# Optimization experiments

Measured on AMD Instinct MI355X. Metric: run time of the kernel, lower is better.

Reference implementation:

```python
import jax, jax.numpy as jnp
import numpy as np
import math

D_MODEL = 64
D_STATE = 16
V_RANGE = 1
K = 3
BATCH, H, W = 4, 32, 32
V_LIST = [(x, y) for x in range(-V_RANGE, V_RANGE + 1) for y in range(-V_RANGE, V_RANGE + 1)]
NUM_V = len(V_LIST)


def _circ_conv(x, w):
    # x: (B, Cin, H, W), w: (Cout, Cin, K, K); circular padding then VALID conv
    p = K // 2
    xp = jnp.pad(x, ((0, 0), (0, 0), (p, p), (p, p)), mode='wrap')
    return jax.lax.conv_general_dilated(
        xp, w, window_strides=(1, 1), padding='VALID',
        dimension_numbers=('NCHW', 'OIHW', 'NCHW'))


def setup_inputs() -> dict:
    key = jax.random.key(0)
    ks = jax.random.split(key, 8)
    fan = 1.0 / math.sqrt(D_MODEL * K * K)
    u_t = jax.random.normal(ks[0], (BATCH, D_MODEL, H, W), dtype=jnp.float32)
    s_prev = jax.random.normal(ks[1], (BATCH, NUM_V, D_MODEL, D_STATE, H, W), dtype=jnp.float32)
    conv_delta_w = jax.random.normal(ks[2], (D_MODEL, D_MODEL, K, K), dtype=jnp.float32) * fan
    conv_delta_b = jax.random.normal(ks[3], (D_MODEL,), dtype=jnp.float32) * 0.01
    conv_B_w = jax.random.normal(ks[4], (D_STATE, D_MODEL, K, K), dtype=jnp.float32) * fan
    conv_C_w = jax.random.normal(ks[5], (D_STATE, D_MODEL, K, K), dtype=jnp.float32) * fan
    log_A_real = jnp.log(0.5 * jnp.ones((D_MODEL, D_STATE), dtype=jnp.float32))
    D = jnp.ones((D_MODEL,), dtype=jnp.float32)
    dt_inv_softplus = jnp.asarray(math.log(math.e - 1.0), dtype=jnp.float32)
    return {
        'u_t': u_t, 's_prev': s_prev,
        'conv_delta_w': conv_delta_w, 'conv_delta_b': conv_delta_b,
        'conv_B_w': conv_B_w, 'conv_C_w': conv_C_w,
        'log_A_real': log_A_real, 'D': D, 'dt_inv_softplus': dt_inv_softplus,
    }


def reference(u_t, s_prev, conv_delta_w, conv_delta_b, conv_B_w, conv_C_w,
              log_A_real, D, dt_inv_softplus):
    # delta: (B, d_model, h, w)
    delta = jax.nn.softplus(_circ_conv(u_t, conv_delta_w)
                            + conv_delta_b[None, :, None, None] + dt_inv_softplus)
    B_val = _circ_conv(u_t, conv_B_w)   # (B, d_state, h, w)
    C_val = _circ_conv(u_t, conv_C_w)   # (B, d_state, h, w)
    A = -jnp.exp(log_A_real)            # (d_model, d_state)
    A_bc = A[None, :, :, None, None]    # (1, d_model, d_state, 1, 1)
    A_bar = jnp.exp(delta[:, :, None] * A_bc)        # (B, d_model, d_state, h, w)
    B_bar = (A_bar - 1.0) / A_bc * B_val[:, None]    # (B, d_model, d_state, h, w)
    u_bc = u_t[:, :, None]              # (B, d_model, 1, h, w)
    C_bc = C_val[:, None]               # (B, 1, d_state, h, w)
    y_skip = u_t * D[None, :, None, None]

    s_next_list, y_list = [], []
    for i, (vx, vy) in enumerate(V_LIST):
        s_tr = jnp.roll(s_prev[:, i], shift=(-vy, -vx), axis=(-2, -1))
        s_new = A_bar * s_tr + B_bar * u_bc          # (B, d_model, d_state, h, w)
        y_new = jnp.sum(s_new * C_bc, axis=2) + y_skip
        s_next_list.append(s_new)
        y_list.append(y_new)
    s_next = jnp.stack(s_next_list, axis=1)  # (B, num_v, d_model, d_state, h, w)
    y_out = jnp.stack(y_list, axis=1)        # (B, num_v, d_model, h, w)
    return (y_out, s_next)
```

## Files before the change

kernel.cpp:

```cpp
#include <hip/hip_runtime.h>
#include <math.h>

#define NBATCH 4
#define NV 9
#define DM 64
#define DS 16

__device__ __forceinline__ float softplus_f(float x) {
    return (x > 20.f) ? x : log1pf(__expf(x));
}

__global__ __launch_bounds__(256) void conv_kernel(
    const float* __restrict__ u, const float* __restrict__ wd,
    const float* __restrict__ bd, const float* __restrict__ wb,
    const float* __restrict__ wc, const float* __restrict__ dtp,
    float* __restrict__ delta_out, float* __restrict__ Bv_out,
    float* __restrict__ Cv_out)
{
    int bx = blockIdx.x;
    int ht = bx & 3;
    int co = (bx >> 2) % 96;
    int b  = bx / 384;
    int tid = threadIdx.x;
    int chunk = __builtin_amdgcn_readfirstlane(tid >> 6);
    int pxt = tid & 63;
    int row = ht * 8 + (pxt >> 3);
    int w0  = (pxt & 7) << 2;

    const float* wbase = (co < 64) ? (wd + (size_t)co * 576)
                       : (co < 80) ? (wb + (size_t)(co - 64) * 576)
                                   : (wc + (size_t)(co - 80) * 576);

    int hm = (row + 31) & 31, hp = (row + 1) & 31;
    int wl = (w0 + 31) & 31;
    int wr = (w0 + 4) & 31;
    const float* ub = u + (size_t)b * 65536 + (size_t)(chunk << 4) * 1024;
    const float* wq0 = wbase + (size_t)(chunk << 4) * 9;

    float a0 = 0.f, a1 = 0.f, a2 = 0.f, a3 = 0.f;
    #pragma unroll 4
    for (int j = 0; j < 16; ++j) {
        const float* base = ub + j * 1024;
        const float* wq = wq0 + j * 9;
        #pragma unroll
        for (int r = 0; r < 3; ++r) {
            int rr = (r == 0) ? hm : (r == 1) ? row : hp;
            const float* rp = base + rr * 32;
            float4 v = *(const float4*)(rp + w0);
            float L = rp[wl], R = rp[wr];
            float k0 = wq[r * 3 + 0], k1 = wq[r * 3 + 1], k2 = wq[r * 3 + 2];
            a0 = fmaf(k0, L,   fmaf(k1, v.x, fmaf(k2, v.y, a0)));
            a1 = fmaf(k0, v.x, fmaf(k1, v.y, fmaf(k2, v.z, a1)));
            a2 = fmaf(k0, v.y, fmaf(k1, v.z, fmaf(k2, v.w, a2)));
            a3 = fmaf(k0, v.z, fmaf(k1, v.w, fmaf(k2, R,   a3)));
        }
    }

    __shared__ float4 part[4][64];
    part[chunk][pxt] = make_float4(a0, a1, a2, a3);
    __syncthreads();

    if (tid < 64) {
        float4 p0 = part[0][tid], p1 = part[1][tid];
        float4 p2 = part[2][tid], p3 = part[3][tid];
        float s0 = p0.x + p1.x + p2.x + p3.x;
        float s1 = p0.y + p1.y + p2.y + p3.y;
        float s2 = p0.z + p1.z + p2.z + p3.z;
        float s3 = p0.w + p1.w + p2.w + p3.w;
        int prow = ht * 8 + (tid >> 3);
        int pw   = (tid & 7) << 2;
        int pix  = prow * 32 + pw;
        if (co < 64) {
            float bias = bd[co] + dtp[0];
            float4 o;
            o.x = softplus_f(s0 + bias);
            o.y = softplus_f(s1 + bias);
            o.z = softplus_f(s2 + bias);
            o.w = softplus_f(s3 + bias);
            *(float4*)(delta_out + (((size_t)b * 64 + co) << 10) + pix) = o;
        } else if (co < 80) {
            *(float4*)(Bv_out + (((size_t)b * 16 + (co - 64)) << 10) + pix) =
                make_float4(s0, s1, s2, s3);
        } else {
            *(float4*)(Cv_out + (((size_t)b * 16 + (co - 80)) << 10) + pix) =
                make_float4(s0, s1, s2, s3);
        }
    }
}

__global__ __launch_bounds__(256) void scan_kernel(
    const float* __restrict__ u, const float* __restrict__ s_prev,
    const float* __restrict__ logA, const float* __restrict__ Dp,
    const float* __restrict__ delta_in, const float* __restrict__ Bv,
    const float* __restrict__ Cv,
    float* __restrict__ y_out, float* __restrict__ s_next)
{
    int bx = blockIdx.x;
    int t  = bx & 3;
    int c  = (bx >> 2) & 63;
    int bi = bx >> 8;
    int i  = bi % 9;
    int b  = bi / 9;

    int tid = threadIdx.x;
    int pix = (t << 8) + tid;
    int h = pix >> 5, w = pix & 31;

    int vx = i / 3 - 1;
    int vy = i % 3 - 1;
    int hh = (h + vy + 32) & 31;
    int ww = (w + vx + 32) & 31;

    __shared__ float sA[16], srA[16];
    if (tid < 16) {
        float A = -__expf(logA[c * 16 + tid]);
        sA[tid]  = A;
        srA[tid] = __builtin_amdgcn_rcpf(A);
    }
    __syncthreads();

    size_t ub = (((size_t)b * 64 + c) << 10) + pix;
    float uv = u[ub];
    float dv = delta_in[ub];
    float y  = uv * Dp[c];

    const float* bvp = Bv + ((size_t)b << 14) + pix;
    const float* cvp = Cv + ((size_t)b << 14) + pix;

    float ab[16], bu[16], cc[16];
    #pragma unroll
    for (int n = 0; n < 16; ++n) {
        float A = sA[n];
        float e = __expf(dv * A);
        ab[n] = e;
        bu[n] = (e - 1.0f) * srA[n] * bvp[(size_t)n << 10] * uv;
        cc[n] = cvp[(size_t)n << 10];
    }

    size_t chan = (((size_t)bi * 64 + c) << 4);
    const float* sp = s_prev + (chan << 10) + hh * 32 + ww;
    float*       sn = s_next + (chan << 10) + pix;

    float sv[16];
    #pragma unroll
    for (int n = 0; n < 16; ++n)
        sv[n] = sp[(size_t)n << 10];

    #pragma unroll
    for (int n = 0; n < 16; ++n) {
        float v = fmaf(ab[n], sv[n], bu[n]);
        __builtin_nontemporal_store(v, sn + ((size_t)n << 10));
        y = fmaf(v, cc[n], y);
    }
    __builtin_nontemporal_store(y, y_out + (((size_t)bi * 64 + c) << 10) + pix);
}

extern "C" void kernel_launch(void* const* d_in, const int* in_sizes, int n_in,
                              void* d_out, int out_size, void* d_ws, size_t ws_size,
                              hipStream_t stream) {
    const float* u      = (const float*)d_in[0];
    const float* s_prev = (const float*)d_in[1];
    const float* wd     = (const float*)d_in[2];
    const float* bd     = (const float*)d_in[3];
    const float* wb     = (const float*)d_in[4];
    const float* wc     = (const float*)d_in[5];
    const float* logA   = (const float*)d_in[6];
    const float* Dp     = (const float*)d_in[7];
    const float* dtp    = (const float*)d_in[8];

    float* ws    = (float*)d_ws;
    float* delta = ws;
    float* Bv    = ws + 262144;
    float* Cv    = ws + 327680;

    float* y_out  = (float*)d_out;
    float* s_next = y_out + (size_t)NBATCH * NV * DM * 1024;

    conv_kernel<<<dim3(4 * 96 * 4), dim3(256), 0, stream>>>(
        u, wd, bd, wb, wc, dtp, delta, Bv, Cv);
    scan_kernel<<<dim3(4 * 9 * 64 * 4), dim3(256), 0, stream>>>(
        u, s_prev, logA, Dp, delta, Bv, Cv, y_out, s_next);
}
```

Measured before the change: 102.6 us.

## Precompute A table in prep kernel and make scan kernel loop over tiles

A tiny prep kernel now computes A=-exp(logA) and its reciprocal once into workspace, which removes the per-block shared-memory setup and __syncthreads from the scan kernel. The scan kernel launches 1536 blocks, each looping over 6 tiles, instead of one block per tile, to cut block launch and setup overhead. The cost is an extra kernel launch and less parallel slack for hiding memory latency, because fewer blocks are resident to cover the loads.

```diff
diff --git a/kernel.cpp b/kernel.cpp
--- a/kernel.cpp
+++ b/kernel.cpp
@@ -8,6 +8,12 @@
 
 __device__ __forceinline__ float softplus_f(float x) {
     return (x > 20.f) ? x : log1pf(__expf(x));
+}
+
+__global__ void prep_kernel(const float* __restrict__ logA, float2* __restrict__ Atab) {
+    int t = threadIdx.x;
+    float A = -__expf(logA[t]);
+    Atab[t] = make_float2(A, __builtin_amdgcn_rcpf(A));
 }
 
 __global__ __launch_bounds__(256) void conv_kernel(
@@ -90,69 +96,65 @@
 
 __global__ __launch_bounds__(256) void scan_kernel(
     const float* __restrict__ u, const float* __restrict__ s_prev,
-    const float* __restrict__ logA, const float* __restrict__ Dp,
+    const float2* __restrict__ Atab, const float* __restrict__ Dp,
     const float* __restrict__ delta_in, const float* __restrict__ Bv,
     const float* __restrict__ Cv,
     float* __restrict__ y_out, float* __restrict__ s_next)
 {
-    int bx = blockIdx.x;
-    int t  = bx & 3;
-    int c  = (bx >> 2) & 63;
-    int bi = bx >> 8;
-    int i  = bi % 9;
-    int b  = bi / 9;
+    const int tid = threadIdx.x;
 
-    int tid = threadIdx.x;
-    int pix = (t << 8) + tid;
-    int h = pix >> 5, w = pix & 31;
+    #pragma unroll 1
+    for (int k = 0; k < 6; ++k) {
+        int tile = blockIdx.x + k * 1536;
+        int t  = tile & 3;
+        int c  = __builtin_amdgcn_readfirstlane((tile >> 2) & 63);
+        int bi = tile >> 8;
+        int i  = bi % 9;
+        int b  = bi / 9;
 
-    int vx = i / 3 - 1;
-    int vy = i % 3 - 1;
-    int hh = (h + vy + 32) & 31;
-    int ww = (w + vx + 32) & 31;
+        int pix = (t << 8) + tid;
+        int h = pix >> 5, w = pix & 31;
+        int vx = i / 3 - 1;
+        int vy = i % 3 - 1;
+        int hh = (h + vy + 32) & 31;
+        int ww = (w + vx + 32) & 31;
 
-    __shared__ float sA[16], srA[16];
-    if (tid < 16) {
-        float A = -__expf(logA[c * 16 + tid]);
-        sA[tid]  = A;
-        srA[tid] = __builtin_amdgcn_rcpf(A);
+        size_t ub = (((size_t)b * 64 + c) << 10) + pix;
+        float uv = u[ub];
+        float dv = delta_in[ub];
+        float y  = uv * Dp[c];
+
+        const float*  bvp = Bv + ((size_t)b << 14) + pix;
+        const float*  cvp = Cv + ((size_t)b << 14) + pix;
+        const float2* at  = Atab + (c << 4);
+
+        float ab[16], bu[16], cc[16];
+        #pragma unroll
+        for (int n = 0; n < 16; ++n) {
+            float2 Ar = at[n];
+            float e = __expf(dv * Ar.x);
+            ab[n] = e;
+            bu[n] = (e - 1.0f) * Ar.y * bvp[(size_t)n << 10] * uv;
+            cc[n] = cvp[(size_t)n << 10];
+        }
+
+        size_t chan = (((size_t)bi * 64 + c) << 4);
+        const float* sp = s_prev + (chan << 10) + hh * 32 + ww;
+        float*       sn = s_next + (chan << 10) + pix;
+
+        float sv[16];
+        #pragma unroll
+        for (int n = 0; n < 16; ++n)
+            sv[n] = sp[(size_t)n << 10];
+
+        #pragma unroll
+        for (int n = 0; n < 16; ++n) {
+            float v = fmaf(ab[n], sv[n], bu[n]);
+            __builtin_nontemporal_store(v, sn + ((size_t)n << 10));
+            y = fmaf(v, cc[n], y);
+        }
+        __builtin_nontemporal_store(y, y_out + (((size_t)bi * 64 + c) << 10) + pix);
     }
-    __syncthreads();
-
-    size_t ub = (((size_t)b * 64 + c) << 10) + pix;
-    float uv = u[ub];
-    float dv = delta_in[ub];
-    float y  = uv * Dp[c];
-
-    const float* bvp = Bv + ((size_t)b << 14) + pix;
-    const float* cvp = Cv + ((size_t)b << 14) + pix;
-
-    float ab[16], bu[16], cc[16];
-    #pragma unroll
-    for (int n = 0; n < 16; ++n) {
-        float A = sA[n];
-        float e = __expf(dv * A);
-        ab[n] = e;
-        bu[n] = (e - 1.0f) * srA[n] * bvp[(size_t)n << 10] * uv;
-        cc[n] = cvp[(size_t)n << 10];
-    }
-
-    size_t chan = (((size_t)bi * 64 + c) << 4);
-    const float* sp = s_prev + (chan << 10) + hh * 32 + ww;
-    float*       sn = s_next + (chan << 10) + pix;
-
-    float sv[16];
-    #pragma unroll
-    for (int n = 0; n < 16; ++n)
-        sv[n] = sp[(size_t)n << 10];
-
-    #pragma unroll
-    for (int n = 0; n < 16; ++n) {
-        float v = fmaf(ab[n], sv[n], bu[n]);
-        __builtin_nontemporal_store(v, sn + ((size_t)n << 10));
-        y = fmaf(v, cc[n], y);
-    }
-    __builtin_nontemporal_store(y, y_out + (((size_t)bi * 64 + c) << 10) + pix);
 }
 
 extern "C" void kernel_launch(void* const* d_in, const int* in_sizes, int n_in,
@@ -172,12 +174,14 @@
     float* delta = ws;
     float* Bv    = ws + 262144;
     float* Cv    = ws + 327680;
+    float2* Atab = (float2*)(ws + 393216);
 
     float* y_out  = (float*)d_out;
     float* s_next = y_out + (size_t)NBATCH * NV * DM * 1024;
 
+    prep_kernel<<<dim3(1), dim3(1024), 0, stream>>>(logA, Atab);
     conv_kernel<<<dim3(4 * 96 * 4), dim3(256), 0, stream>>>(
         u, wd, bd, wb, wc, dtp, delta, Bv, Cv);
-    scan_kernel<<<dim3(4 * 9 * 64 * 4), dim3(256), 0, stream>>>(
-        u, s_prev, logA, Dp, delta, Bv, Cv, y_out, s_next);
+    scan_kernel<<<dim3(1536), dim3(256), 0, stream>>>(
+        u, s_prev, Atab, Dp, delta, Bv, Cv, y_out, s_next);
 }
```

After: 107.8 us. 5.1% more time.
